# Optimization experiments

Measured on AMD Instinct MI355X. Metric: run time of the kernel, lower is better.

The kernel has to match this reference:

```python
import jax, jax.numpy as jnp
import numpy as np

DIM = 768
HEADS = 12
HEAD_DIM = DIM // HEADS
RANK = 8
SCALING = 1.0 / RANK  # lora_alpha / r
SCALE = HEAD_DIM ** -0.5


def setup_inputs() -> dict:
    key = jax.random.key(0)
    ks = jax.random.split(key, 14)
    B, N, D, r = 4, 1024, DIM, RANK
    s = lambda k, shape, sd=0.02: jax.random.normal(k, shape, jnp.float32) * sd
    return {
        "x": jax.random.normal(ks[0], (B, N, D), jnp.float32),
        "qkv_w": s(ks[1], (3 * D, D)),
        "qkv_b": s(ks[2], (3 * D,)),
        "q_base_w": s(ks[3], (D, D)),
        "q_base_b": s(ks[4], (D,)),
        "q_A": s(ks[5], (r, D), 1.0 / r),
        "q_B": s(ks[6], (D, r)),
        "k_base_w": s(ks[7], (D, D)),
        "k_base_b": s(ks[8], (D,)),
        "k_A": s(ks[9], (r, D), 1.0 / r),
        "k_B": s(ks[10], (D, r)),
        "proj_w": s(ks[11], (D, D)),
        "proj_b": s(ks[12], (D,)),
    }


def _lora_linear(x, w, b, A, Bm):
    # base linear + LoRA delta: x@w.T + b + (x@A.T)@B.T * scaling
    return x @ w.T + b + ((x @ A.T) @ Bm.T) * SCALING


def reference(x, qkv_w, qkv_b, q_base_w, q_base_b, q_A, q_B,
              k_base_w, k_base_b, k_A, k_B, proj_w, proj_b):
    B, N, D = x.shape
    H, hd = HEADS, HEAD_DIM
    qkv = (x @ qkv_w.T + qkv_b).reshape(B, N, 3, H, hd).transpose(2, 0, 3, 1, 4)
    q, k, v = qkv[0], qkv[1], qkv[2]  # [B,H,N,hd]
    q_delta = _lora_linear(x, q_base_w, q_base_b, q_A, q_B).reshape(B, N, H, hd).transpose(0, 2, 1, 3)
    k_delta = _lora_linear(x, k_base_w, k_base_b, k_A, k_B).reshape(B, N, H, hd).transpose(0, 2, 1, 3)
    q = q + q_delta
    k = k + k_delta
    attn = jnp.einsum('bhnd,bhmd->bhnm', q, k) * SCALE
    attn = jax.nn.softmax(attn, axis=-1)
    out = jnp.einsum('bhnm,bhmd->bhnd', attn, v)
    out = out.transpose(0, 2, 1, 3).reshape(B, N, D)
    return out @ proj_w.T + proj_b
```

## Files before the change

kernel.cpp:

```cpp
#include <hip/hip_runtime.h>
#include <hip/hip_bf16.h>


typedef _Float16 half8 __attribute__((ext_vector_type(8)));
typedef float f32x4 __attribute__((ext_vector_type(4)));

typedef __attribute__((address_space(3))) unsigned int lds_u32;
typedef __attribute__((address_space(1))) const unsigned int glob_u32;

__device__ __forceinline__ void glds16(const void* g, void* l) {
    __builtin_amdgcn_global_load_lds((glob_u32*)g, (lds_u32*)l, 16, 0, 0);
}

__device__ __forceinline__ float pk2f16(float a, float b) {
    return __builtin_bit_cast(float, __builtin_amdgcn_cvt_pkrtz(a, b));
}

#define SMSCALE 0.18033688011112042f

constexpr size_t OFF_WX = 0;
constexpr size_t OFF_PH = OFF_WX + (size_t)2304*800*2;
constexpr size_t OFF_XE = OFF_PH + (size_t)768*768*2;
constexpr size_t OFF_QH = OFF_XE + (size_t)4096*800*2;
constexpr size_t OFF_KH = OFF_QH + (size_t)48*1024*64*2;
constexpr size_t OFF_VH = OFF_KH + (size_t)48*1024*64*2;
constexpr size_t OFF_VT = OFF_VH + (size_t)48*1024*64*2;
constexpr size_t OFF_AO = OFF_VT + (size_t)48*1024*64*2;

__global__ __launch_bounds__(256)
void prep(const float* __restrict__ qkv_w, const float* __restrict__ qkv_b,
          const float* __restrict__ qw, const float* __restrict__ qbias,
          const float* __restrict__ kw, const float* __restrict__ kbias,
          const float* __restrict__ proj_w, const float* __restrict__ qB,
          const float* __restrict__ kB,
          _Float16* __restrict__ Wx, _Float16* __restrict__ Ph) {
    const int t = threadIdx.x, bb = blockIdx.x;
    if (bb < 2304) {
        const int n = bb;
        const float rs = (n < 768) ? SMSCALE : 1.0f;
        const float* wsrc = qkv_w + (size_t)n * 768;
        const float* fold = (n < 768) ? (qw + (size_t)n * 768)
                          : (n < 1536 ? (kw + (size_t)(n - 768) * 768) : nullptr);
        _Float16* dst = Wx + (size_t)n * 800;
#pragma unroll
        for (int i = 0; i < 3; ++i) {
            const int c = t + i * 256;
            float v = wsrc[c];
            if (fold) v += fold[c];
            dst[c] = (_Float16)(v * rs);
        }
        if (t < 32) {
            float v = 0.f;
            if (t < 8)       { if (n < 768) v = rs * 0.125f * qB[n * 8 + t]; }
            else if (t < 16) { if (n >= 768 && n < 1536) v = 0.125f * kB[(size_t)(n - 768) * 8 + (t - 8)]; }
            else if (t == 16) v = rs * (qkv_b[n] + (n < 768 ? qbias[n] : (n < 1536 ? kbias[n - 768] : 0.f)));
            dst[768 + t] = (_Float16)v;
        }
    } else {
        const size_t idx = ((size_t)(bb - 2304) * 256 + t) * 4;
        const float4 v = *(const float4*)(proj_w + idx);
        _Float16* d = Ph + idx;
        d[0] = (_Float16)v.x; d[1] = (_Float16)v.y;
        d[2] = (_Float16)v.z; d[3] = (_Float16)v.w;
    }
}

__global__ __launch_bounds__(256)
void lora_xa(const float* __restrict__ x, const float* __restrict__ qA,
             const float* __restrict__ kA, _Float16* __restrict__ Xe) {
    __shared__ float xs[768];
    const int m = blockIdx.x, t = threadIdx.x;
    const float* xr = x + (size_t)m * 768;
    _Float16* dst = Xe + (size_t)m * 800;
#pragma unroll
    for (int i = 0; i < 3; ++i) {
        const int c = t + i * 256;
        const float v = xr[c];
        xs[c] = v;
        dst[c] = (_Float16)v;
    }
    __syncthreads();
    const int j = t >> 4, l = t & 15;
    const float* Arow = (j < 8) ? (qA + j * 768) : (kA + (j - 8) * 768);
    float acc = 0.f;
    for (int k = l; k < 768; k += 16) acc += xs[k] * Arow[k];
    acc += __shfl_xor(acc, 1); acc += __shfl_xor(acc, 2);
    acc += __shfl_xor(acc, 4); acc += __shfl_xor(acc, 8);
    if (l == 0) dst[768 + j] = (_Float16)acc;
    if (t >= 240) dst[784 + (t - 240)] = (t == 240) ? (_Float16)1.f : (_Float16)0.f;
}

template<int BM, int BN, int MODE>
__global__ __launch_bounds__(256)
void gemm_h(const _Float16* __restrict__ A, const _Float16* __restrict__ Bw,
            const int lda, const int ldb, const int nsteps,
            const float* __restrict__ bias,
            _Float16* __restrict__ Oq, _Float16* __restrict__ Ok, _Float16* __restrict__ Ov,
            float* __restrict__ Co) {
    constexpr int CA = BM / 16, CB = BN / 16;
    constexpr int MI = BM / 32, NI = BN / 32;
    __shared__ __align__(16) _Float16 As[2][BM * 32];
    __shared__ __align__(16) _Float16 Bs[2][BN * 32];
    const int t = threadIdx.x;
    const int w = t >> 6, l = t & 63;
    const int l15 = l & 15, lg = l >> 4;
    const int wm = w >> 1, wn = w & 1;

    const int gx = gridDim.x;
    int lin = blockIdx.y * gx + blockIdx.x;
    lin = (lin & 7) * ((gx * gridDim.y) >> 3) + (lin >> 3);
    const int n0 = (lin % gx) * BN, m0 = (lin / gx) * BM;

    const _Float16* gA[CA / 4];
    const _Float16* gB[CB / 4];
#pragma unroll
    for (int i = 0; i < CA / 4; ++i)
        gA[i] = A + (size_t)(m0 + (w * (CA / 4) + i) * 16 + l15) * lda + lg * 8;
#pragma unroll
    for (int i = 0; i < CB / 4; ++i)
        gB[i] = Bw + (size_t)(n0 + (w * (CB / 4) + i) * 16 + l15) * ldb + lg * 8;

    f32x4 acc[MI][NI];
#pragma unroll
    for (int mi = 0; mi < MI; ++mi)
#pragma unroll
        for (int ni = 0; ni < NI; ++ni) acc[mi][ni] = 0.f;

#pragma unroll
    for (int i = 0; i < CA / 4; ++i) { glds16(gA[i], &As[0][(w * (CA / 4) + i) * 512]); gA[i] += 32; }
#pragma unroll
    for (int i = 0; i < CB / 4; ++i) { glds16(gB[i], &Bs[0][(w * (CB / 4) + i) * 512]); gB[i] += 32; }
    __syncthreads();

    for (int s = 0; s < nsteps; ++s) {
        const int cur = s & 1;
        if (s + 1 < nsteps) {
#pragma unroll
            for (int i = 0; i < CA / 4; ++i) { glds16(gA[i], &As[cur ^ 1][(w * (CA / 4) + i) * 512]); gA[i] += 32; }
#pragma unroll
            for (int i = 0; i < CB / 4; ++i) { glds16(gB[i], &Bs[cur ^ 1][(w * (CB / 4) + i) * 512]); gB[i] += 32; }
        }
        half8 a[MI], b[NI];
#pragma unroll
        for (int mi = 0; mi < MI; ++mi) a[mi] = *(const half8*)&As[cur][(wm * MI + mi) * 512 + l * 8];
#pragma unroll
        for (int ni = 0; ni < NI; ++ni) b[ni] = *(const half8*)&Bs[cur][(wn * NI + ni) * 512 + l * 8];
#pragma unroll
        for (int mi = 0; mi < MI; ++mi)
#pragma unroll
            for (int ni = 0; ni < NI; ++ni)
                acc[mi][ni] = __builtin_amdgcn_mfma_f32_16x16x32_f16(a[mi], b[ni], acc[mi][ni], 0, 0, 0);
        __syncthreads();
    }

    if (MODE == 0) {
#pragma unroll
        for (int mi = 0; mi < MI; ++mi)
#pragma unroll
            for (int reg = 0; reg < 4; ++reg) {
                const int m = m0 + wm * (BM / 2) + mi * 16 + lg * 4 + reg;
                const int b_ = m >> 10, nn = m & 1023;
#pragma unroll
                for (int ni = 0; ni < NI; ++ni) {
                    const int n = n0 + wn * (BN / 2) + ni * 16 + l15;
                    const int sel = (n >= 1536) ? 2 : (n >= 768 ? 1 : 0);
                    const int jj = n - sel * 768;
                    const int h = jj >> 6, d = jj & 63;
                    _Float16* dst = (sel == 0) ? Oq : (sel == 1 ? Ok : Ov);
                    dst[(((size_t)(b_ * 12 + h)) * 1024 + nn) * 64 + d] = (_Float16)acc[mi][ni][reg];
                }
            }
    } else {
#pragma unroll
        for (int mi = 0; mi < MI; ++mi)
#pragma unroll
            for (int reg = 0; reg < 4; ++reg) {
                const int m = m0 + wm * (BM / 2) + mi * 16 + lg * 4 + reg;
#pragma unroll
                for (int ni = 0; ni < NI; ++ni) {
                    const int n = n0 + wn * (BN / 2) + ni * 16 + l15;
                    Co[(size_t)m * 768 + n] = acc[mi][ni][reg] + bias[n];
                }
            }
    }
}

__global__ __launch_bounds__(256)
void vt_k(const _Float16* __restrict__ Vh, _Float16* __restrict__ Vt) {
    __shared__ __align__(16) _Float16 tile[64][72];
    const int t = threadIdx.x;
    const int nb = blockIdx.x, bh = blockIdx.y;
    {
        const int key = t >> 2, h0 = (t & 3) * 16;
        const size_t src = ((size_t)(bh * 1024 + nb * 64 + key)) * 64 + h0;
        *(half8*)&tile[key][h0]     = *(const half8*)&Vh[src];
        *(half8*)&tile[key][h0 + 8] = *(const half8*)&Vh[src + 8];
    }
    __syncthreads();
    const int hd = t >> 2, k0 = (t & 3) * 16;
    half8 a, b;
#pragma unroll
    for (int j = 0; j < 8; ++j) { a[j] = tile[k0 + j][hd]; b[j] = tile[k0 + 8 + j][hd]; }
    const size_t dst = ((size_t)(bh * 64 + hd)) * 1024 + nb * 64 + k0;
    *(half8*)&Vt[dst]     = a;
    *(half8*)&Vt[dst + 8] = b;
}

__global__ __launch_bounds__(128)
void attn2(const _Float16* __restrict__ Q, const _Float16* __restrict__ K,
           const _Float16* __restrict__ Vt, _Float16* __restrict__ AO) {
    __shared__ __align__(16) _Float16 Ks[2][4096];
    __shared__ __align__(16) _Float16 Vs[2][4096];
    __shared__ __align__(16) _Float16 Ps[2][2048];
    __shared__ float sums[2][32];
    const int t = threadIdx.x;
    const int w = t >> 6, l = t & 63;
    const int l15 = l & 15, lg = l >> 4;

    int lin = blockIdx.y * 16 + blockIdx.x;
    lin = (lin & 7) * 96 + (lin >> 3);
    const int qb = lin & 15, bh = lin >> 4;

    const _Float16* Qp = Q  + (size_t)bh * 65536;
    const _Float16* Kp = K  + (size_t)bh * 65536;
    const _Float16* Vp = Vt + (size_t)bh * 65536;

#pragma unroll
    for (int i = 0; i < 4; ++i) {
        const int c = w * 4 + i;
        glds16(Kp + (size_t)((c >> 1) * 16 + l15) * 64 + (c & 1) * 32 + lg * 8, &Ks[0][c * 512]);
        glds16(Vp + (size_t)((c >> 1) * 16 + l15) * 1024 + (c & 1) * 32 + lg * 8, &Vs[0][c * 512]);
    }
    half8 qf[2][2];
#pragma unroll
    for (int mi = 0; mi < 2; ++mi)
#pragma unroll
        for (int kh = 0; kh < 2; ++kh)
            qf[mi][kh] = *(const half8*)&Qp[(size_t)(qb * 64 + w * 32 + mi * 16 + l15) * 64 + kh * 32 + lg * 8];

    f32x4 o[2][4];
#pragma unroll
    for (int mi = 0; mi < 2; ++mi)
#pragma unroll
        for (int fj = 0; fj < 4; ++fj) o[mi][fj] = 0.f;
    float lsum[2] = {0.f, 0.f};
    __syncthreads();

    for (int kb = 0; kb < 16; ++kb) {
        const int cur = kb & 1;
        if (kb < 15) {
#pragma unroll
            for (int i = 0; i < 4; ++i) {
                const int c = w * 4 + i;
                glds16(Kp + (size_t)((kb + 1) * 64 + (c >> 1) * 16 + l15) * 64 + (c & 1) * 32 + lg * 8,
                       &Ks[cur ^ 1][c * 512]);
                glds16(Vp + (size_t)((c >> 1) * 16 + l15) * 1024 + (kb + 1) * 64 + (c & 1) * 32 + lg * 8,
                       &Vs[cur ^ 1][c * 512]);
            }
        }

        half8 kreg[8];
#pragma unroll
        for (int c = 0; c < 8; ++c) kreg[c] = *(const half8*)&Ks[cur][c * 512 + l * 8];

#pragma unroll
        for (int mi = 0; mi < 2; ++mi) {
            f32x4 s[4];
#pragma unroll
            for (int nj = 0; nj < 4; ++nj) s[nj] = 0.f;
#pragma unroll
            for (int nj = 0; nj < 4; ++nj)
#pragma unroll
                for (int kh = 0; kh < 2; ++kh)
                    s[nj] = __builtin_amdgcn_mfma_f32_16x16x32_f16(kreg[nj * 2 + kh], qf[mi][kh], s[nj], 0, 0, 0);
            float ls = 0.f;
#pragma unroll
            for (int nj = 0; nj < 4; ++nj) {
                const float p0 = __builtin_amdgcn_exp2f(s[nj][0]);
                const float p1 = __builtin_amdgcn_exp2f(s[nj][1]);
                const float p2 = __builtin_amdgcn_exp2f(s[nj][2]);
                const float p3 = __builtin_amdgcn_exp2f(s[nj][3]);
                ls += (p0 + p1) + (p2 + p3);
                float2 pk;
                pk.x = pk2f16(p0, p1);
                pk.y = pk2f16(p2, p3);
                const int off = (mi * 2 + (nj >> 1)) * 512 + (2 * (nj & 1) + (lg >> 1)) * 128
                              + l15 * 8 + 4 * (lg & 1);
                *(float2*)&Ps[w][off] = pk;
            }
            lsum[mi] += ls;
        }

        half8 pf[2][2];
#pragma unroll
        for (int mi = 0; mi < 2; ++mi)
#pragma unroll
            for (int kh = 0; kh < 2; ++kh)
                pf[mi][kh] = *(const half8*)&Ps[w][(mi * 2 + kh) * 512 + l * 8];

#pragma unroll
        for (int fj = 0; fj < 4; ++fj)
#pragma unroll
            for (int kh = 0; kh < 2; ++kh) {
                const half8 vf = *(const half8*)&Vs[cur][(fj * 2 + kh) * 512 + l * 8];
#pragma unroll
                for (int mi = 0; mi < 2; ++mi)
                    o[mi][fj] = __builtin_amdgcn_mfma_f32_16x16x32_f16(pf[mi][kh], vf, o[mi][fj], 0, 0, 0);
            }
        __syncthreads();
    }

#pragma unroll
    for (int mi = 0; mi < 2; ++mi) {
        float tot = lsum[mi];
        tot += __shfl_xor(tot, 16);
        tot += __shfl_xor(tot, 32);
        if (lg == 0) sums[w][mi * 16 + l15] = tot;
    }
    __builtin_amdgcn_wave_barrier();

    const int b_ = bh / 12, h = bh % 12;
#pragma unroll
    for (int mi = 0; mi < 2; ++mi)
#pragma unroll
        for (int reg = 0; reg < 4; ++reg) {
            const float inv = 1.f / sums[w][mi * 16 + lg * 4 + reg];
            const int tok = qb * 64 + w * 32 + mi * 16 + lg * 4 + reg;
            const size_t base = ((size_t)(b_ * 1024 + tok)) * 768 + h * 64;
#pragma unroll
            for (int fj = 0; fj < 4; ++fj)
                AO[base + fj * 16 + l15] = (_Float16)(o[mi][fj][reg] * inv);
        }
}

extern "C" void kernel_launch(void* const* d_in, const int* in_sizes, int n_in,
                              void* d_out, int out_size, void* d_ws, size_t ws_size,
                              hipStream_t stream) {
    (void)in_sizes; (void)n_in; (void)out_size; (void)ws_size;
    const float* x      = (const float*)d_in[0];
    const float* qkv_w  = (const float*)d_in[1];
    const float* qkv_b  = (const float*)d_in[2];
    const float* q_bw   = (const float*)d_in[3];
    const float* q_bb   = (const float*)d_in[4];
    const float* q_A    = (const float*)d_in[5];
    const float* q_B    = (const float*)d_in[6];
    const float* k_bw   = (const float*)d_in[7];
    const float* k_bb   = (const float*)d_in[8];
    const float* k_A    = (const float*)d_in[9];
    const float* k_B    = (const float*)d_in[10];
    const float* proj_w = (const float*)d_in[11];
    const float* proj_b = (const float*)d_in[12];
    float* out = (float*)d_out;
    char*  ws  = (char*)d_ws;

    _Float16* Wx = (_Float16*)(ws + OFF_WX);
    _Float16* Ph = (_Float16*)(ws + OFF_PH);
    _Float16* Xe = (_Float16*)(ws + OFF_XE);
    _Float16* Qh = (_Float16*)(ws + OFF_QH);
    _Float16* Kh = (_Float16*)(ws + OFF_KH);
    _Float16* Vh = (_Float16*)(ws + OFF_VH);
    _Float16* Vt = (_Float16*)(ws + OFF_VT);
    _Float16* AO = (_Float16*)(ws + OFF_AO);

    prep<<<dim3(2880), dim3(256), 0, stream>>>(qkv_w, qkv_b, q_bw, q_bb, k_bw, k_bb,
                                               proj_w, q_B, k_B, Wx, Ph);
    lora_xa<<<dim3(4096), dim3(256), 0, stream>>>(x, q_A, k_A, Xe);
    gemm_h<128, 128, 0><<<dim3(18, 32), dim3(256), 0, stream>>>(
        Xe, Wx, 800, 800, 25, nullptr, Qh, Kh, Vh, nullptr);
    vt_k<<<dim3(16, 48), dim3(256), 0, stream>>>(Vh, Vt);
    attn2<<<dim3(16, 48), dim3(128), 0, stream>>>(Qh, Kh, Vt, AO);
    gemm_h<64, 128, 1><<<dim3(6, 64), dim3(256), 0, stream>>>(
        AO, Ph, 768, 768, 24, proj_b, nullptr, nullptr, nullptr, out);
}
```

Before: 115.6 us.

## Load K/V fragments directly into registers with double-buffered prefetch in attention

The attention kernel stops staging K and V tiles in shared memory via global_load_lds with block barriers. Each wave now reads its MFMA fragments straight from global memory into two register buffers, prefetching the next key block while computing the current one, and the loop is unrolled by two. This removes LDS traffic and the per-iteration __syncthreads. In exchange both waves fetch the same K/V data separately, which doubles global/L2 reads, and the register buffers raise VGPR pressure. A launch-bounds hint of two blocks per CU is also added.

New measurement: 129.9 us. 1.12x slower.

```diff
diff --git a/kernel.cpp b/kernel.cpp
--- a/kernel.cpp
+++ b/kernel.cpp
@@ -206,11 +206,63 @@
     *(half8*)&Vt[dst + 8] = b;
 }
 
-__global__ __launch_bounds__(128)
-void attn2(const _Float16* __restrict__ Q, const _Float16* __restrict__ K,
+#define LOADK(dst, kbt) { \
+_Pragma("unroll") \
+    for (int c = 0; c < 8; ++c) \
+        dst[c] = *(const half8*)(Kp + (size_t)((kbt) * 64 + (c >> 1) * 16 + l15) * 64 + (c & 1) * 32 + lg * 8); }
+
+#define LOADV(dst, kbt) { \
+_Pragma("unroll") \
+    for (int c = 0; c < 8; ++c) \
+        dst[c] = *(const half8*)(Vp + (size_t)((c >> 1) * 16 + l15) * 1024 + (kbt) * 64 + (c & 1) * 32 + lg * 8); }
+
+#define STEP(kreg, vreg) { \
+_Pragma("unroll") \
+    for (int mi = 0; mi < 2; ++mi) { \
+        f32x4 s[4]; \
+_Pragma("unroll") \
+        for (int nj = 0; nj < 4; ++nj) s[nj] = 0.f; \
+_Pragma("unroll") \
+        for (int nj = 0; nj < 4; ++nj) \
+_Pragma("unroll") \
+            for (int kh = 0; kh < 2; ++kh) \
+                s[nj] = __builtin_amdgcn_mfma_f32_16x16x32_f16(kreg[nj * 2 + kh], qf[mi][kh], s[nj], 0, 0, 0); \
+        float ls = 0.f; \
+_Pragma("unroll") \
+        for (int nj = 0; nj < 4; ++nj) { \
+            const float p0 = __builtin_amdgcn_exp2f(s[nj][0]); \
+            const float p1 = __builtin_amdgcn_exp2f(s[nj][1]); \
+            const float p2 = __builtin_amdgcn_exp2f(s[nj][2]); \
+            const float p3 = __builtin_amdgcn_exp2f(s[nj][3]); \
+            ls += (p0 + p1) + (p2 + p3); \
+            float2 pk; \
+            pk.x = pk2f16(p0, p1); \
+            pk.y = pk2f16(p2, p3); \
+            const int off = (mi * 2 + (nj >> 1)) * 512 + (2 * (nj & 1) + (lg >> 1)) * 128 \
+                          + l15 * 8 + 4 * (lg & 1); \
+            *(float2*)&Ps[w][off] = pk; \
+        } \
+        lsum[mi] += ls; \
+    } \
+    { \
+        half8 pf[2][2]; \
+_Pragma("unroll") \
+        for (int mi = 0; mi < 2; ++mi) \
+_Pragma("unroll") \
+            for (int kh = 0; kh < 2; ++kh) \
+                pf[mi][kh] = *(const half8*)&Ps[w][(mi * 2 + kh) * 512 + l * 8]; \
+_Pragma("unroll") \
+        for (int fj = 0; fj < 4; ++fj) \
+_Pragma("unroll") \
+            for (int kh = 0; kh < 2; ++kh) \
+_Pragma("unroll") \
+                for (int mi = 0; mi < 2; ++mi) \
+                    o[mi][fj] = __builtin_amdgcn_mfma_f32_16x16x32_f16(pf[mi][kh], vreg[fj * 2 + kh], o[mi][fj], 0, 0, 0); \
+    } }
+
+__global__ __launch_bounds__(128, 2)
+void attn3(const _Float16* __restrict__ Q, const _Float16* __restrict__ K,
            const _Float16* __restrict__ Vt, _Float16* __restrict__ AO) {
-    __shared__ __align__(16) _Float16 Ks[2][4096];
-    __shared__ __align__(16) _Float16 Vs[2][4096];
     __shared__ __align__(16) _Float16 Ps[2][2048];
     __shared__ float sums[2][32];
     const int t = threadIdx.x;
@@ -225,12 +277,6 @@
     const _Float16* Kp = K  + (size_t)bh * 65536;
     const _Float16* Vp = Vt + (size_t)bh * 65536;
 
-#pragma unroll
-    for (int i = 0; i < 4; ++i) {
-        const int c = w * 4 + i;
-        glds16(Kp + (size_t)((c >> 1) * 16 + l15) * 64 + (c & 1) * 32 + lg * 8, &Ks[0][c * 512]);
-        glds16(Vp + (size_t)((c >> 1) * 16 + l15) * 1024 + (c & 1) * 32 + lg * 8, &Vs[0][c * 512]);
-    }
     half8 qf[2][2];
 #pragma unroll
     for (int mi = 0; mi < 2; ++mi)
@@ -244,70 +290,16 @@
 #pragma unroll
         for (int fj = 0; fj < 4; ++fj) o[mi][fj] = 0.f;
     float lsum[2] = {0.f, 0.f};
-    __syncthreads();
-
-    for (int kb = 0; kb < 16; ++kb) {
-        const int cur = kb & 1;
-        if (kb < 15) {
-#pragma unroll
-            for (int i = 0; i < 4; ++i) {
-                const int c = w * 4 + i;
-                glds16(Kp + (size_t)((kb + 1) * 64 + (c >> 1) * 16 + l15) * 64 + (c & 1) * 32 + lg * 8,
-                       &Ks[cur ^ 1][c * 512]);
-                glds16(Vp + (size_t)((c >> 1) * 16 + l15) * 1024 + (kb + 1) * 64 + (c & 1) * 32 + lg * 8,
-                       &Vs[cur ^ 1][c * 512]);
-            }
-        }
-
-        half8 kreg[8];
-#pragma unroll
-        for (int c = 0; c < 8; ++c) kreg[c] = *(const half8*)&Ks[cur][c * 512 + l * 8];
-
-#pragma unroll
-        for (int mi = 0; mi < 2; ++mi) {
-            f32x4 s[4];
-#pragma unroll
-            for (int nj = 0; nj < 4; ++nj) s[nj] = 0.f;
-#pragma unroll
-            for (int nj = 0; nj < 4; ++nj)
-#pragma unroll
-                for (int kh = 0; kh < 2; ++kh)
-                    s[nj] = __builtin_amdgcn_mfma_f32_16x16x32_f16(kreg[nj * 2 + kh], qf[mi][kh], s[nj], 0, 0, 0);
-            float ls = 0.f;
-#pragma unroll
-            for (int nj = 0; nj < 4; ++nj) {
-                const float p0 = __builtin_amdgcn_exp2f(s[nj][0]);
-                const float p1 = __builtin_amdgcn_exp2f(s[nj][1]);
-                const float p2 = __builtin_amdgcn_exp2f(s[nj][2]);
-                const float p3 = __builtin_amdgcn_exp2f(s[nj][3]);
-                ls += (p0 + p1) + (p2 + p3);
-                float2 pk;
-                pk.x = pk2f16(p0, p1);
-                pk.y = pk2f16(p2, p3);
-                const int off = (mi * 2 + (nj >> 1)) * 512 + (2 * (nj & 1) + (lg >> 1)) * 128
-                              + l15 * 8 + 4 * (lg & 1);
-                *(float2*)&Ps[w][off] = pk;
-            }
-            lsum[mi] += ls;
-        }
-
-        half8 pf[2][2];
-#pragma unroll
-        for (int mi = 0; mi < 2; ++mi)
-#pragma unroll
-            for (int kh = 0; kh < 2; ++kh)
-                pf[mi][kh] = *(const half8*)&Ps[w][(mi * 2 + kh) * 512 + l * 8];
-
-#pragma unroll
-        for (int fj = 0; fj < 4; ++fj)
-#pragma unroll
-            for (int kh = 0; kh < 2; ++kh) {
-                const half8 vf = *(const half8*)&Vs[cur][(fj * 2 + kh) * 512 + l * 8];
-#pragma unroll
-                for (int mi = 0; mi < 2; ++mi)
-                    o[mi][fj] = __builtin_amdgcn_mfma_f32_16x16x32_f16(pf[mi][kh], vf, o[mi][fj], 0, 0, 0);
-            }
-        __syncthreads();
+
+    half8 kfa[8], vfa[8], kfb[8], vfb[8];
+    LOADK(kfa, 0); LOADV(vfa, 0);
+
+    for (int it = 0; it < 8; ++it) {
+        const int k0 = it * 2;
+        LOADK(kfb, k0 + 1); LOADV(vfb, k0 + 1);
+        STEP(kfa, vfa);
+        if (it < 7) { LOADK(kfa, k0 + 2); LOADV(vfa, k0 + 2); }
+        STEP(kfb, vfb);
     }
 
 #pragma unroll
@@ -368,7 +360,7 @@
     gemm_h<128, 128, 0><<<dim3(18, 32), dim3(256), 0, stream>>>(
         Xe, Wx, 800, 800, 25, nullptr, Qh, Kh, Vh, nullptr);
     vt_k<<<dim3(16, 48), dim3(256), 0, stream>>>(Vh, Vt);
-    attn2<<<dim3(16, 48), dim3(128), 0, stream>>>(Qh, Kh, Vt, AO);
+    attn3<<<dim3(16, 48), dim3(128), 0, stream>>>(Qh, Kh, Vt, AO);
     gemm_h<64, 128, 1><<<dim3(6, 64), dim3(256), 0, stream>>>(
         AO, Ph, 768, 768, 24, proj_b, nullptr, nullptr, nullptr, out);
 }
```
